# Kernel tuning notes

Hardware: AMD Instinct MI355X
Metric: run time of the kernel (lower is better)

## Reference

```python
import jax, jax.numpy as jnp
import numpy as np
import math

DIM = 1024
NHEADS = 8
HEAD_DIM = 128
MAXSEQLEN = 2048
THETA = 10000.0


def _rope_tables():
    # speed = theta ** (-(arange(0, dim, 2) / dim)), t = arange(maxseqlen)
    half = HEAD_DIM // 2
    speed = THETA ** (-(np.arange(0, HEAD_DIM, 2)[:half].astype(np.float32) / HEAD_DIM))
    t = np.arange(MAXSEQLEN, dtype=np.float32)
    freqs = np.outer(t, speed)  # [maxseqlen, head_dim//2]
    return jnp.asarray(np.cos(freqs)), jnp.asarray(np.sin(freqs))


def setup_inputs() -> dict:
    key = jax.random.key(0)
    kx, kqkv, kout = jax.random.split(key, 3)
    B, T = 2, 2048
    hdim = NHEADS * HEAD_DIM
    std = 0.5 * DIM ** (-0.5)
    bound = (3.0 ** 0.5) * std
    x = jax.random.normal(kx, (B, T, DIM), dtype=jnp.float32)
    qkv_proj = jax.random.uniform(kqkv, (3, hdim, DIM), dtype=jnp.float32,
                                  minval=-bound, maxval=bound)
    # nn.Linear(hdim, dim, bias=False) default init: U(-1/sqrt(hdim), 1/sqrt(hdim))
    wb = 1.0 / math.sqrt(hdim)
    w_out = jax.random.uniform(kout, (DIM, hdim), dtype=jnp.float32,
                               minval=-wb, maxval=wb)
    cos, sin = _rope_tables()
    return {"x": x, "qkv_proj": qkv_proj, "w_out": w_out, "cos": cos, "sin": sin}


def _apply_rope(u, cos, sin):
    # u: [B, T, H, D]; rotate adjacent pairs (complex multiply)
    B, T, H, D = u.shape
    u = u.reshape(B, T, H, D // 2, 2)
    c = cos[:T][None, :, None, :]  # [1, T, 1, D//2]
    s = sin[:T][None, :, None, :]
    re = u[..., 0] * c - u[..., 1] * s
    im = u[..., 0] * s + u[..., 1] * c
    return jnp.stack([re, im], axis=-1).reshape(B, T, H, D)


def reference(x, qkv_proj, w_out, cos, sin):
    B, T, D = x.shape
    # fused QKV projection: [B, T, 3, hdim] -> [B, T, 3, H, head_dim]
    qkv = jnp.einsum('btd,ahd->btah', x, qkv_proj)
    qkv = qkv.reshape(B, T, 3, NHEADS, HEAD_DIM)
    q, k, v = qkv[:, :, 0], qkv[:, :, 1], qkv[:, :, 2]
    q = _apply_rope(q, cos, sin)
    k = _apply_rope(k, cos, sin)
    scale = HEAD_DIM ** (-0.5)
    logits = jnp.einsum('btnh,bsnh->bnts', q, k) * scale  # [B, H, T, T]
    causal = jnp.tril(jnp.ones((T, T), dtype=bool))
    masked = jnp.where(causal[None, None], logits, -jnp.inf)
    attn = jax.nn.softmax(masked, axis=-1)
    out = jnp.einsum('bnts,bsnh->btnh', attn, v).reshape(B, T, -1)
    out = out @ w_out.T  # [B, T, dim]
    return out, attn
```

## Files before the change

### kernel.cpp

```cpp
#include <hip/hip_runtime.h>

typedef __attribute__((ext_vector_type(8))) short bf16x8;
typedef __attribute__((ext_vector_type(4))) short bf16x4;
typedef __attribute__((ext_vector_type(4))) float f32x4;

#define MFMA(a, b, c) __builtin_amdgcn_mfma_f32_16x16x32_bf16((a), (b), (c), 0, 0, 0)

__device__ __forceinline__ unsigned short f2bf(float f) {
  unsigned int x = __float_as_uint(f);
  return (unsigned short)((x + 0x7fffu + ((x >> 16) & 1u)) >> 16);
}

constexpr int SEQ = 2048;
constexpr int NH = 8;
constexpr int DH = 128;
constexpr int DIM = 1024;
constexpr float SCALE = 0.08838834764831845f;

__global__ __launch_bounds__(256) void k_qkv_rope(
    const float* __restrict__ x, const float* __restrict__ wqkv,
    const float* __restrict__ cosT, const float* __restrict__ sinT,
    unsigned short* __restrict__ q, unsigned short* __restrict__ k,
    unsigned short* __restrict__ vT)
{
  __shared__ __align__(16) unsigned short As[128][40];
  __shared__ __align__(16) unsigned short Bs[128][40];
  const int tid = threadIdx.x;
  const int wave = tid >> 6, lane = tid & 63;
  const int fr = lane & 15, fq = lane >> 4;
  const int fk = fq * 8;
  const int wr = (wave >> 1) * 64, wc = (wave & 1) * 64;
  const int m0 = blockIdx.x * 128, n0 = blockIdx.y * 128;

  f32x4 zero4 = {0.f, 0.f, 0.f, 0.f};
  f32x4 acc[4][4];
  for (int i = 0; i < 4; ++i)
    for (int j = 0; j < 4; ++j) acc[i][j] = zero4;

  for (int kt = 0; kt < 32; ++kt) {
    const int k0 = kt * 32;
    __syncthreads();
#pragma unroll
    for (int j = 0; j < 4; ++j) {
      int f = j * 256 + tid;
      int row = f >> 3, c4 = (f & 7) * 4;
      f32x4 va = *(const f32x4*)(x + (m0 + row) * 1024 + k0 + c4);
      f32x4 vb = *(const f32x4*)(wqkv + (n0 + row) * 1024 + k0 + c4);
      bf16x4 ha, hb;
#pragma unroll
      for (int e = 0; e < 4; ++e) {
        ha[e] = (short)f2bf(va[e]);
        hb[e] = (short)f2bf(vb[e]);
      }
      *(bf16x4*)&As[row][c4] = ha;
      *(bf16x4*)&Bs[row][c4] = hb;
    }
    __syncthreads();
    bf16x8 af[4], bfr[4];
#pragma unroll
    for (int mi = 0; mi < 4; ++mi) af[mi] = *(const bf16x8*)&As[wr + mi * 16 + fr][fk];
#pragma unroll
    for (int ni = 0; ni < 4; ++ni) bfr[ni] = *(const bf16x8*)&Bs[wc + ni * 16 + fr][fk];
#pragma unroll
    for (int mi = 0; mi < 4; ++mi)
#pragma unroll
      for (int ni = 0; ni < 4; ++ni)
        acc[mi][ni] = MFMA(af[mi], bfr[ni], acc[mi][ni]);
  }

#pragma unroll
  for (int mi = 0; mi < 4; ++mi)
#pragma unroll
    for (int ni = 0; ni < 4; ++ni)
#pragma unroll
      for (int r = 0; r < 4; ++r) {
        float val = acc[mi][ni][r];
        float other = __shfl_xor(val, 1, 64);
        int m = m0 + wr + mi * 16 + fq * 4 + r;
        int n = n0 + wc + ni * 16 + fr;
        int a = n >> 10, feat = n & 1023;
        int hh = feat >> 7, dh = feat & 127;
        int bi = m >> 11, t = m & 2047;
        if (a == 2) {
          vT[((bi * NH + hh) * DH + dh) * SEQ + t] = f2bf(val);
        } else {
          float c = cosT[t * 64 + (dh >> 1)];
          float s = sinT[t * 64 + (dh >> 1)];
          float o = ((dh & 1) == 0) ? (val * c - other * s) : (other * s + val * c);
          unsigned short* dst = (a == 0) ? q : k;
          dst[((bi * NH + hh) * SEQ + t) * DH + dh] = f2bf(o);
        }
      }
}

__global__ __launch_bounds__(256) void k_attn(
    const unsigned short* __restrict__ q, const unsigned short* __restrict__ k,
    const unsigned short* __restrict__ vT,
    float* __restrict__ attn, unsigned short* __restrict__ heads)
{
  __shared__ __align__(16) unsigned short Kt[32][136];
  __shared__ __align__(16) unsigned short Vt[128][40];
  __shared__ __align__(16) unsigned short Esc[4][16][40];

  const int tid = threadIdx.x;
  const int wave = tid >> 6, lane = tid & 63;
  const int fr = lane & 15, fq = lane >> 4;
  const int fk = fq * 8;
  const int rt = (blockIdx.z == 0) ? (int)blockIdx.x : (31 - (int)blockIdx.x);
  const int row0 = rt * 64;
  const int hh = blockIdx.y, bi = blockIdx.z;
  const int bh = bi * NH + hh;
  const int r0 = row0 + wave * 16;

  const unsigned short* qb = q + bh * SEQ * DH;
  const unsigned short* kb = k + bh * SEQ * DH;
  const unsigned short* vb = vT + bh * DH * SEQ;

  bf16x8 aq[4];
#pragma unroll
  for (int ks = 0; ks < 4; ++ks)
    aq[ks] = *(const bf16x8*)(qb + (r0 + fr) * DH + ks * 32 + fk);

  const int ntile = row0 / 32 + 2;
  const int wmax = r0 + 15;

  float rs[4] = {0.f, 0.f, 0.f, 0.f};

  for (int nt = 0; nt < ntile; ++nt) {
    const int c0 = nt * 32;
    __syncthreads();
#pragma unroll
    for (int j = 0; j < 2; ++j) {
      int f = j * 256 + tid;
      int r = f >> 4, c = (f & 15) * 8;
      *(bf16x8*)&Kt[r][c] = *(const bf16x8*)(kb + (c0 + r) * DH + c);
    }
    __syncthreads();
    if (c0 <= wmax) {
#pragma unroll
      for (int half = 0; half < 2; ++half) {
        f32x4 s = {0.f, 0.f, 0.f, 0.f};
#pragma unroll
        for (int ks = 0; ks < 4; ++ks) {
          bf16x8 bk = *(const bf16x8*)&Kt[half * 16 + fr][ks * 32 + fk];
          s = MFMA(aq[ks], bk, s);
        }
        int col = c0 + half * 16 + fr;
#pragma unroll
        for (int r = 0; r < 4; ++r) {
          int row = r0 + fq * 4 + r;
          if (col <= row) rs[r] += __expf(s[r] * SCALE);
        }
      }
    }
  }

#pragma unroll
  for (int r = 0; r < 4; ++r)
#pragma unroll
    for (int msk = 1; msk < 16; msk <<= 1)
      rs[r] += __shfl_xor(rs[r], msk, 64);

  float inv[4];
#pragma unroll
  for (int r = 0; r < 4; ++r) inv[r] = 1.0f / rs[r];

  f32x4 pv[8];
  {
    f32x4 zero4 = {0.f, 0.f, 0.f, 0.f};
#pragma unroll
    for (int i = 0; i < 8; ++i) pv[i] = zero4;
  }

  for (int nt = 0; nt < ntile; ++nt) {
    const int c0 = nt * 32;
    __syncthreads();
#pragma unroll
    for (int j = 0; j < 2; ++j) {
      int f = j * 256 + tid;
      int r = f >> 4, c = (f & 15) * 8;
      *(bf16x8*)&Kt[r][c] = *(const bf16x8*)(kb + (c0 + r) * DH + c);
      int rv = f >> 2, cv = (f & 3) * 8;
      *(bf16x8*)&Vt[rv][cv] = *(const bf16x8*)(vb + rv * SEQ + c0 + cv);
    }
    __syncthreads();
    if (c0 <= wmax) {
#pragma unroll
      for (int half = 0; half < 2; ++half) {
        f32x4 s = {0.f, 0.f, 0.f, 0.f};
#pragma unroll
        for (int ks = 0; ks < 4; ++ks) {
          bf16x8 bk = *(const bf16x8*)&Kt[half * 16 + fr][ks * 32 + fk];
          s = MFMA(aq[ks], bk, s);
        }
        int col = c0 + half * 16 + fr;
#pragma unroll
        for (int r = 0; r < 4; ++r) {
          int row = r0 + fq * 4 + r;
          float p = (col <= row) ? __expf(s[r] * SCALE) * inv[r] : 0.f;
          attn[((size_t)bh * SEQ + row) * SEQ + col] = p;
          Esc[wave][fq * 4 + r][half * 16 + fr] = f2bf(p);
        }
      }
      bf16x8 ae = *(const bf16x8*)&Esc[wave][fr][fk];
#pragma unroll
      for (int ni = 0; ni < 8; ++ni) {
        bf16x8 bv = *(const bf16x8*)&Vt[ni * 16 + fr][fk];
        pv[ni] = MFMA(ae, bv, pv[ni]);
      }
    }
  }

#pragma unroll
  for (int ni = 0; ni < 8; ++ni)
#pragma unroll
    for (int r = 0; r < 4; ++r) {
      int row = r0 + fq * 4 + r;
      int dh = ni * 16 + fr;
      heads[(bi * SEQ + row) * DIM + hh * DH + dh] = f2bf(pv[ni][r]);
    }

  {
    const int zstart = row0 + ((wave >= 2) ? 64 : 32);
    f32x4 z4 = {0.f, 0.f, 0.f, 0.f};
#pragma unroll
    for (int rr = 0; rr < 4; ++rr) {
      int row = r0 + rr * 4 + fq;
      float* dst = attn + ((size_t)bh * SEQ + row) * SEQ;
      for (int c = zstart + fr * 4; c < SEQ; c += 64)
        *(f32x4*)(dst + c) = z4;
    }
  }
}

__global__ __launch_bounds__(256) void k_outproj(
    const unsigned short* __restrict__ heads, const float* __restrict__ wout,
    float* __restrict__ out)
{
  __shared__ __align__(16) unsigned short As[128][40];
  __shared__ __align__(16) unsigned short Bs[128][40];
  const int tid = threadIdx.x;
  const int wave = tid >> 6, lane = tid & 63;
  const int fr = lane & 15, fq = lane >> 4;
  const int fk = fq * 8;
  const int wr = (wave >> 1) * 64, wc = (wave & 1) * 64;
  const int m0 = blockIdx.x * 128, n0 = blockIdx.y * 128;

  f32x4 zero4 = {0.f, 0.f, 0.f, 0.f};
  f32x4 acc[4][4];
  for (int i = 0; i < 4; ++i)
    for (int j = 0; j < 4; ++j) acc[i][j] = zero4;

  for (int kt = 0; kt < 32; ++kt) {
    const int k0 = kt * 32;
    __syncthreads();
#pragma unroll
    for (int j = 0; j < 2; ++j) {
      int f = j * 256 + tid;
      int row = f >> 2, c = (f & 3) * 8;
      *(bf16x8*)&As[row][c] = *(const bf16x8*)(heads + (m0 + row) * 1024 + k0 + c);
    }
#pragma unroll
    for (int j = 0; j < 4; ++j) {
      int f = j * 256 + tid;
      int row = f >> 3, c4 = (f & 7) * 4;
      f32x4 vb = *(const f32x4*)(wout + (n0 + row) * 1024 + k0 + c4);
      bf16x4 hb;
#pragma unroll
      for (int e = 0; e < 4; ++e) hb[e] = (short)f2bf(vb[e]);
      *(bf16x4*)&Bs[row][c4] = hb;
    }
    __syncthreads();
    bf16x8 af[4], bfr[4];
#pragma unroll
    for (int mi = 0; mi < 4; ++mi) af[mi] = *(const bf16x8*)&As[wr + mi * 16 + fr][fk];
#pragma unroll
    for (int ni = 0; ni < 4; ++ni) bfr[ni] = *(const bf16x8*)&Bs[wc + ni * 16 + fr][fk];
#pragma unroll
    for (int mi = 0; mi < 4; ++mi)
#pragma unroll
      for (int ni = 0; ni < 4; ++ni)
        acc[mi][ni] = MFMA(af[mi], bfr[ni], acc[mi][ni]);
  }

#pragma unroll
  for (int mi = 0; mi < 4; ++mi)
#pragma unroll
    for (int ni = 0; ni < 4; ++ni)
#pragma unroll
      for (int r = 0; r < 4; ++r) {
        int m = m0 + wr + mi * 16 + fq * 4 + r;
        int n = n0 + wc + ni * 16 + fr;
        out[m * 1024 + n] = acc[mi][ni][r];
      }
}

extern "C" void kernel_launch(void* const* d_in, const int* in_sizes, int n_in,
                              void* d_out, int out_size, void* d_ws, size_t ws_size,
                              hipStream_t stream)
{
  const float* x    = (const float*)d_in[0];
  const float* wqkv = (const float*)d_in[1];
  const float* wout = (const float*)d_in[2];
  const float* cosT = (const float*)d_in[3];
  const float* sinT = (const float*)d_in[4];

  float* out  = (float*)d_out;
  float* attn = out + 4194304;
  unsigned short* ws   = (unsigned short*)d_ws;
  unsigned short* q     = ws;
  unsigned short* kk    = ws + 4194304;
  unsigned short* vT    = ws + 8388608;
  unsigned short* heads = ws + 12582912;

  k_qkv_rope<<<dim3(32, 24), 256, 0, stream>>>(x, wqkv, cosT, sinT, q, kk, vT);
  k_attn<<<dim3(32, 8, 2), 256, 0, stream>>>(q, kk, vT, attn, heads);
  k_outproj<<<dim3(32, 8), 256, 0, stream>>>(heads, wout, out);
}
```

Measured before the change: 241.8 us.

## Widen attention key tiles to 64 and use packed bf16 conversion instruction

The attention kernel now processes 64 key columns per tile instead of 32, with per-16-column liveness masking, so it needs half as many tile iterations and barriers and does two PV MFMAs per tile. Shared-memory row padding is adjusted for the wider tiles. Separately, the fp32-to-bf16 conversions in the QKV and output-projection GEMMs switch from a manual rounding sequence to the hardware v_cvt_pk_bf16_f32 instruction. Wider tiles raise shared-memory use, and masked diagonal blocks still issue stores and zero-probability PV MFMAs.

```diff
diff --git a/kernel.cpp b/kernel.cpp
--- a/kernel.cpp
+++ b/kernel.cpp
@@ -9,6 +9,11 @@
 __device__ __forceinline__ unsigned short f2bf(float f) {
   unsigned int x = __float_as_uint(f);
   return (unsigned short)((x + 0x7fffu + ((x >> 16) & 1u)) >> 16);
+}
+__device__ __forceinline__ unsigned int cvtpk(float lo, float hi) {
+  unsigned int r;
+  asm("v_cvt_pk_bf16_f32 %0, %1, %2" : "=v"(r) : "v"(lo), "v"(hi));
+  return r;
 }
 
 constexpr int SEQ = 2048;
@@ -46,14 +51,11 @@
       int row = f >> 3, c4 = (f & 7) * 4;
       f32x4 va = *(const f32x4*)(x + (m0 + row) * 1024 + k0 + c4);
       f32x4 vb = *(const f32x4*)(wqkv + (n0 + row) * 1024 + k0 + c4);
-      bf16x4 ha, hb;
-#pragma unroll
-      for (int e = 0; e < 4; ++e) {
-        ha[e] = (short)f2bf(va[e]);
-        hb[e] = (short)f2bf(vb[e]);
-      }
-      *(bf16x4*)&As[row][c4] = ha;
-      *(bf16x4*)&Bs[row][c4] = hb;
+      uint2 ua, ub;
+      ua.x = cvtpk(va[0], va[1]); ua.y = cvtpk(va[2], va[3]);
+      ub.x = cvtpk(vb[0], vb[1]); ub.y = cvtpk(vb[2], vb[3]);
+      *(uint2*)&As[row][c4] = ua;
+      *(uint2*)&Bs[row][c4] = ub;
     }
     __syncthreads();
     bf16x8 af[4], bfr[4];
@@ -98,9 +100,9 @@
     const unsigned short* __restrict__ vT,
     float* __restrict__ attn, unsigned short* __restrict__ heads)
 {
-  __shared__ __align__(16) unsigned short Kt[32][136];
-  __shared__ __align__(16) unsigned short Vt[128][40];
-  __shared__ __align__(16) unsigned short Esc[4][16][40];
+  __shared__ __align__(16) unsigned short Kt[64][140];
+  __shared__ __align__(16) unsigned short Vt[128][76];
+  __shared__ __align__(16) unsigned short Esc[4][16][76];
 
   const int tid = threadIdx.x;
   const int wave = tid >> 6, lane = tid & 63;
@@ -121,31 +123,30 @@
   for (int ks = 0; ks < 4; ++ks)
     aq[ks] = *(const bf16x8*)(qb + (r0 + fr) * DH + ks * 32 + fk);
 
-  const int ntile = row0 / 32 + 2;
   const int wmax = r0 + 15;
-
   float rs[4] = {0.f, 0.f, 0.f, 0.f};
 
-  for (int nt = 0; nt < ntile; ++nt) {
-    const int c0 = nt * 32;
-    __syncthreads();
-#pragma unroll
-    for (int j = 0; j < 2; ++j) {
+  for (int nt = 0; nt <= rt; ++nt) {
+    const int c0 = nt * 64;
+    __syncthreads();
+#pragma unroll
+    for (int j = 0; j < 4; ++j) {
       int f = j * 256 + tid;
       int r = f >> 4, c = (f & 15) * 8;
       *(bf16x8*)&Kt[r][c] = *(const bf16x8*)(kb + (c0 + r) * DH + c);
     }
     __syncthreads();
-    if (c0 <= wmax) {
-#pragma unroll
-      for (int half = 0; half < 2; ++half) {
+#pragma unroll
+    for (int half = 0; half < 4; ++half) {
+      int ch = c0 + half * 16;
+      if (ch <= wmax) {
         f32x4 s = {0.f, 0.f, 0.f, 0.f};
 #pragma unroll
         for (int ks = 0; ks < 4; ++ks) {
           bf16x8 bk = *(const bf16x8*)&Kt[half * 16 + fr][ks * 32 + fk];
           s = MFMA(aq[ks], bk, s);
         }
-        int col = c0 + half * 16 + fr;
+        int col = ch + fr;
 #pragma unroll
         for (int r = 0; r < 4; ++r) {
           int row = r0 + fq * 4 + r;
@@ -172,42 +173,47 @@
     for (int i = 0; i < 8; ++i) pv[i] = zero4;
   }
 
-  for (int nt = 0; nt < ntile; ++nt) {
-    const int c0 = nt * 32;
-    __syncthreads();
-#pragma unroll
-    for (int j = 0; j < 2; ++j) {
+  for (int nt = 0; nt <= rt; ++nt) {
+    const int c0 = nt * 64;
+    __syncthreads();
+#pragma unroll
+    for (int j = 0; j < 4; ++j) {
       int f = j * 256 + tid;
       int r = f >> 4, c = (f & 15) * 8;
       *(bf16x8*)&Kt[r][c] = *(const bf16x8*)(kb + (c0 + r) * DH + c);
-      int rv = f >> 2, cv = (f & 3) * 8;
+      int rv = f >> 3, cv = (f & 7) * 8;
       *(bf16x8*)&Vt[rv][cv] = *(const bf16x8*)(vb + rv * SEQ + c0 + cv);
     }
     __syncthreads();
-    if (c0 <= wmax) {
-#pragma unroll
-      for (int half = 0; half < 2; ++half) {
-        f32x4 s = {0.f, 0.f, 0.f, 0.f};
+#pragma unroll
+    for (int half = 0; half < 4; ++half) {
+      int ch = c0 + half * 16;
+      bool live = (ch <= wmax);
+      f32x4 s = {0.f, 0.f, 0.f, 0.f};
+      if (live) {
 #pragma unroll
         for (int ks = 0; ks < 4; ++ks) {
           bf16x8 bk = *(const bf16x8*)&Kt[half * 16 + fr][ks * 32 + fk];
           s = MFMA(aq[ks], bk, s);
         }
-        int col = c0 + half * 16 + fr;
-#pragma unroll
-        for (int r = 0; r < 4; ++r) {
-          int row = r0 + fq * 4 + r;
-          float p = (col <= row) ? __expf(s[r] * SCALE) * inv[r] : 0.f;
-          attn[((size_t)bh * SEQ + row) * SEQ + col] = p;
-          Esc[wave][fq * 4 + r][half * 16 + fr] = f2bf(p);
-        }
-      }
-      bf16x8 ae = *(const bf16x8*)&Esc[wave][fr][fk];
-#pragma unroll
-      for (int ni = 0; ni < 8; ++ni) {
-        bf16x8 bv = *(const bf16x8*)&Vt[ni * 16 + fr][fk];
-        pv[ni] = MFMA(ae, bv, pv[ni]);
-      }
+      }
+      int col = ch + fr;
+#pragma unroll
+      for (int r = 0; r < 4; ++r) {
+        int row = r0 + fq * 4 + r;
+        float p = (live && col <= row) ? __expf(s[r] * SCALE) * inv[r] : 0.f;
+        attn[((size_t)bh * SEQ + row) * SEQ + col] = p;
+        Esc[wave][fq * 4 + r][half * 16 + fr] = f2bf(p);
+      }
+    }
+    bf16x8 ae0 = *(const bf16x8*)&Esc[wave][fr][fk];
+    bf16x8 ae1 = *(const bf16x8*)&Esc[wave][fr][32 + fk];
+#pragma unroll
+    for (int ni = 0; ni < 8; ++ni) {
+      bf16x8 bv0 = *(const bf16x8*)&Vt[ni * 16 + fr][fk];
+      bf16x8 bv1 = *(const bf16x8*)&Vt[ni * 16 + fr][32 + fk];
+      pv[ni] = MFMA(ae0, bv0, pv[ni]);
+      pv[ni] = MFMA(ae1, bv1, pv[ni]);
     }
   }
 
@@ -221,7 +227,7 @@
     }
 
   {
-    const int zstart = row0 + ((wave >= 2) ? 64 : 32);
+    const int zstart = row0 + 64;
     f32x4 z4 = {0.f, 0.f, 0.f, 0.f};
 #pragma unroll
     for (int rr = 0; rr < 4; ++rr) {
@@ -265,10 +271,9 @@
       int f = j * 256 + tid;
       int row = f >> 3, c4 = (f & 7) * 4;
       f32x4 vb = *(const f32x4*)(wout + (n0 + row) * 1024 + k0 + c4);
-      bf16x4 hb;
-#pragma unroll
-      for (int e = 0; e < 4; ++e) hb[e] = (short)f2bf(vb[e]);
-      *(bf16x4*)&Bs[row][c4] = hb;
+      uint2 ub;
+      ub.x = cvtpk(vb[0], vb[1]); ub.y = cvtpk(vb[2], vb[3]);
+      *(uint2*)&Bs[row][c4] = ub;
     }
     __syncthreads();
     bf16x8 af[4], bfr[4];
```

After: 219.7 us. 1.1x faster.
